# Performance work log

Hardware: AMD Instinct MI355X
Metric: run time of the kernel (lower is better)

## Reference

```python
import jax, jax.numpy as jnp
import numpy as np

D_MODEL, D_K, D_V, H = 1024, 64, 64, 16


def setup_inputs() -> dict:
    key = jax.random.key(0)
    ks = jax.random.split(key, 11)
    b, nq, nk = 2, 2048, 2048
    queries = jax.random.normal(ks[0], (b, nq, D_MODEL), dtype=jnp.float32)
    keys = jax.random.normal(ks[1], (b, nk, D_MODEL), dtype=jnp.float32)
    values = jax.random.normal(ks[2], (b, nk, D_MODEL), dtype=jnp.float32)
    def xavier(k, shape):
        fan_in, fan_out = shape[1], shape[0]
        lim = np.sqrt(6.0 / (fan_in + fan_out)).astype(np.float32)
        return jax.random.uniform(k, shape, jnp.float32, -lim, lim)
    # torch Linear weight shape: (out_features, in_features)
    Wq = xavier(ks[3], (H * D_K, D_MODEL)); bq = jnp.zeros((H * D_K,), jnp.float32)
    Wk = xavier(ks[4], (H * D_K, D_MODEL)); bk = jnp.zeros((H * D_K,), jnp.float32)
    Wv = xavier(ks[5], (H * D_V, D_MODEL)); bv = jnp.zeros((H * D_V,), jnp.float32)
    Wo = xavier(ks[6], (D_MODEL, H * D_V)); bo = jnp.zeros((D_MODEL,), jnp.float32)
    return {"queries": queries, "keys": keys, "values": values,
            "Wq": Wq, "bq": bq, "Wk": Wk, "bk": bk,
            "Wv": Wv, "bv": bv, "Wo": Wo, "bo": bo}


def reference(queries, keys, values, Wq, bq, Wk, bk, Wv, bv, Wo, bo):
    b, nq, _ = queries.shape
    nk = keys.shape[1]
    scale = 1.0 / np.sqrt(D_K).astype(np.float32)
    # projections -> (b, h, n, d)
    q = (queries @ Wq.T + bq).reshape(b, nq, H, D_K).transpose(0, 2, 1, 3)
    k = (keys @ Wk.T + bk).reshape(b, nk, H, D_K).transpose(0, 2, 1, 3)
    v = (values @ Wv.T + bv).reshape(b, nk, H, D_V).transpose(0, 2, 1, 3)
    att = jnp.einsum('bhqd,bhkd->bhqk', q, k) * scale  # (b,h,nq,nk)
    att = jax.nn.softmax(att, axis=-1)
    out = jnp.einsum('bhqk,bhkd->bhqd', att, v)        # (b,h,nq,dv)
    out = out.transpose(0, 2, 1, 3).reshape(b, nq, H * D_V)
    return out @ Wo.T + bo
```

## Files before the change

kernel.cpp:

```cpp
#include <hip/hip_runtime.h>
#include <stdint.h>

typedef __bf16 v8bf __attribute__((ext_vector_type(8)));
typedef float  v4f  __attribute__((ext_vector_type(4)));

#define QSCALE 0.18033688011112042f

typedef __attribute__((address_space(3))) void lds_vp;
typedef const __attribute__((address_space(1))) void gbl_vp;
__device__ __forceinline__ void gl_lds16(const __bf16* g, __bf16* l) {
    __builtin_amdgcn_global_load_lds((gbl_vp*)g, (lds_vp*)l, 16, 0, 0);
}

__device__ __forceinline__ v8bf cvt8(const float* __restrict__ p) {
    float4 x = *reinterpret_cast<const float4*>(p);
    float4 y = *reinterpret_cast<const float4*>(p + 4);
    v8bf r;
    r[0] = (__bf16)x.x; r[1] = (__bf16)x.y; r[2] = (__bf16)x.z; r[3] = (__bf16)x.w;
    r[4] = (__bf16)y.x; r[5] = (__bf16)y.y; r[6] = (__bf16)y.z; r[7] = (__bf16)y.w;
    return r;
}

__global__ __launch_bounds__(256) void cvt_w(
    const float* __restrict__ w0, const float* __restrict__ w1,
    const float* __restrict__ w2, const float* __restrict__ w3,
    __bf16* __restrict__ o0, __bf16* __restrict__ o1,
    __bf16* __restrict__ o2, __bf16* __restrict__ o3)
{
    const float* src; __bf16* dst;
    switch (blockIdx.y) {
        case 0: src = w0; dst = o0; break;
        case 1: src = w1; dst = o1; break;
        case 2: src = w2; dst = o2; break;
        default: src = w3; dst = o3; break;
    }
    size_t i = ((size_t)blockIdx.x * 256 + threadIdx.x) * 8;
    *reinterpret_cast<v8bf*>(dst + i) = cvt8(src + i);
}

__global__ __launch_bounds__(256) void cvt_in(
    const float* __restrict__ i0, const float* __restrict__ i1,
    const float* __restrict__ i2,
    __bf16* __restrict__ o0, __bf16* __restrict__ o1, __bf16* __restrict__ o2)
{
    const float* src; __bf16* dst;
    switch (blockIdx.y) {
        case 0: src = i0; dst = o0; break;
        case 1: src = i1; dst = o1; break;
        default: src = i2; dst = o2; break;
    }
    size_t i = ((size_t)blockIdx.x * 256 + threadIdx.x) * 8;
    *reinterpret_cast<v8bf*>(dst + i) = cvt8(src + i);
}

__device__ __forceinline__ void gemm_body(
    const __bf16* __restrict__ A, const __bf16* __restrict__ W,
    const float* __restrict__ bias, void* __restrict__ outp,
    int mode, float oscale, int bx, int by)
{
    constexpr int K = 1024, N = 1024;
    __shared__ __align__(16) __bf16 As[2][128 * 64];
    __shared__ __align__(16) __bf16 Bs[2][64 * 64];

    const int lane = threadIdx.x & 63;
    const int wave = threadIdx.x >> 6;
    const int quad = lane >> 4;
    const int l15  = lane & 15;
    const int m_base = bx * 128;
    const int n_base = by * 64;
    const int wm = (wave & 1) * 64;
    const int wn = (wave >> 1) * 32;

    int arow[4], acol[4], brow[2], bcol[2];
    #pragma unroll
    for (int i = 0; i < 4; ++i) {
        int L = (i * 4 + wave) * 64 + lane;
        int r = L >> 3, s = L & 7;
        arow[i] = r; acol[i] = (s ^ (r & 7)) * 8;
    }
    #pragma unroll
    for (int i = 0; i < 2; ++i) {
        int L = (i * 4 + wave) * 64 + lane;
        int r = L >> 3, s = L & 7;
        brow[i] = r; bcol[i] = (s ^ (r & 7)) * 8;
    }

    v4f acc[4][2];
    #pragma unroll
    for (int f = 0; f < 4; ++f)
        #pragma unroll
        for (int g = 0; g < 2; ++g) { v4f z = {0.f,0.f,0.f,0.f}; acc[f][g] = z; }

    #pragma unroll
    for (int i = 0; i < 4; ++i)
        gl_lds16(A + (size_t)(m_base + arow[i]) * K + acol[i],
                 &As[0][(i * 4 + wave) * 512]);
    #pragma unroll
    for (int i = 0; i < 2; ++i)
        gl_lds16(W + (size_t)(n_base + brow[i]) * K + bcol[i],
                 &Bs[0][(i * 4 + wave) * 512]);
    __syncthreads();

    for (int it = 0; it < 16; ++it) {
        const int cur = it & 1, nxt = cur ^ 1;
        const int kn = ((it + 1) & 15) * 64;
        #pragma unroll
        for (int i = 0; i < 4; ++i)
            gl_lds16(A + (size_t)(m_base + arow[i]) * K + kn + acol[i],
                     &As[nxt][(i * 4 + wave) * 512]);
        #pragma unroll
        for (int i = 0; i < 2; ++i)
            gl_lds16(W + (size_t)(n_base + brow[i]) * K + kn + bcol[i],
                     &Bs[nxt][(i * 4 + wave) * 512]);

        #pragma unroll
        for (int ks = 0; ks < 2; ++ks) {
            v8bf af[4], bf[2];
            #pragma unroll
            for (int f = 0; f < 4; ++f) {
                const int R = wm + f * 16 + l15;
                const int slot = (ks * 4 + quad) ^ (R & 7);
                af[f] = *reinterpret_cast<const v8bf*>(&As[cur][R * 64 + slot * 8]);
            }
            #pragma unroll
            for (int g = 0; g < 2; ++g) {
                const int R = wn + g * 16 + l15;
                const int slot = (ks * 4 + quad) ^ (R & 7);
                bf[g] = *reinterpret_cast<const v8bf*>(&Bs[cur][R * 64 + slot * 8]);
            }
            __builtin_amdgcn_s_setprio(1);
            #pragma unroll
            for (int f = 0; f < 4; ++f)
                #pragma unroll
                for (int g = 0; g < 2; ++g)
                    acc[f][g] = __builtin_amdgcn_mfma_f32_16x16x32_bf16(
                        af[f], bf[g], acc[f][g], 0, 0, 0);
            __builtin_amdgcn_s_setprio(0);
        }
        __syncthreads();
    }

    #pragma unroll
    for (int f = 0; f < 4; ++f)
        #pragma unroll
        for (int g = 0; g < 2; ++g) {
            const int nc = n_base + wn + g * 16 + l15;
            const float bval = bias[nc];
            #pragma unroll
            for (int r = 0; r < 4; ++r) {
                const int m = m_base + wm + f * 16 + quad * 4 + r;
                const float v = (acc[f][g][r] + bval) * oscale;
                if (mode == 2) {
                    ((float*)outp)[(size_t)m * N + nc] = v;
                } else {
                    int b = m >> 11, n = m & 2047, h = nc >> 6, d = nc & 63;
                    size_t off = (mode == 0)
                        ? ((size_t)(b * 16 + h) * 2048 + n) * 64 + d
                        : ((size_t)(b * 16 + h) * 64 + d) * 2048 + n;
                    ((__bf16*)outp)[off] = (__bf16)v;
                }
            }
        }
}

__global__ __launch_bounds__(256) void qkv_gemm(
    const __bf16* __restrict__ Aq, const __bf16* __restrict__ Ak,
    const __bf16* __restrict__ Av,
    const __bf16* __restrict__ Wq, const __bf16* __restrict__ Wk,
    const __bf16* __restrict__ Wv,
    const float* __restrict__ bq, const float* __restrict__ bk,
    const float* __restrict__ bv,
    __bf16* __restrict__ Qo, __bf16* __restrict__ Ko, __bf16* __restrict__ Vo)
{
    const int id = blockIdx.x;
    const int by = id & 15;
    const int bx = (id >> 4) & 31;
    const int z  = id >> 9;

    const __bf16 *A, *W; const float* bias; __bf16* outp; float oscale; int mode;
    switch (z) {
        case 0:  A = Aq; W = Wq; bias = bq; outp = Qo; oscale = QSCALE; mode = 0; break;
        case 1:  A = Ak; W = Wk; bias = bk; outp = Ko; oscale = 1.0f;   mode = 0; break;
        default: A = Av; W = Wv; bias = bv; outp = Vo; oscale = 1.0f;   mode = 1; break;
    }
    gemm_body(A, W, bias, outp, mode, oscale, bx, by);
}

__global__ __launch_bounds__(256) void out_gemm(
    const __bf16* __restrict__ A, const __bf16* __restrict__ W,
    const float* __restrict__ bias, float* __restrict__ outp)
{
    const int by = blockIdx.x & 15;
    const int bx = blockIdx.x >> 4;
    gemm_body(A, W, bias, outp, 2, 1.0f, bx, by);
}

__global__ __launch_bounds__(512, 4) void attn_kernel(
    const __bf16* __restrict__ Q, const __bf16* __restrict__ Kb_,
    const __bf16* __restrict__ Vt, __bf16* __restrict__ O)
{
    __shared__ __align__(16) __bf16 Ks[3][64 * 64];
    __shared__ __align__(16) __bf16 Vs[3][64 * 64];
    __shared__ __align__(16) __bf16 p_lds[8][16][72];

    const int lane = threadIdx.x & 63;
    const int wave = threadIdx.x >> 6;
    const int quad = lane >> 4;
    const int l15  = lane & 15;
    const int bh = blockIdx.x & 31;
    const int qt = blockIdx.x >> 5;
    const int b  = bh >> 4, h = bh & 15;

    const __bf16* Qh = Q   + (size_t)bh * 2048 * 64;
    const __bf16* Kh = Kb_ + (size_t)bh * 2048 * 64;
    const __bf16* Vh = Vt  + (size_t)bh * 64 * 2048;

    const int L    = wave * 64 + lane;
    const int srow = L >> 3;
    const int scol = ((L & 7) ^ (srow & 7)) * 8;

    v8bf qf[2];
    #pragma unroll
    for (int ks = 0; ks < 2; ++ks)
        qf[ks] = *reinterpret_cast<const v8bf*>(
            Qh + (size_t)(qt * 128 + wave * 16 + l15) * 64 + ks * 32 + quad * 8);

    v4f o_acc[4];
    #pragma unroll
    for (int c = 0; c < 4; ++c) { v4f z = {0.f,0.f,0.f,0.f}; o_acc[c] = z; }
    float l_r[4] = {0.f, 0.f, 0.f, 0.f};

    gl_lds16(Kh + (size_t)srow * 64 + scol, &Ks[0][L * 8]);
    gl_lds16(Vh + (size_t)srow * 2048 + scol, &Vs[0][L * 8]);
    gl_lds16(Kh + (size_t)(64 + srow) * 64 + scol, &Ks[1][L * 8]);
    gl_lds16(Vh + (size_t)srow * 2048 + 64 + scol, &Vs[1][L * 8]);
    asm volatile("s_waitcnt vmcnt(2)" ::: "memory");
    __builtin_amdgcn_s_barrier();

    int cur = 0;
    for (int kt = 0; kt < 32; ++kt) {
        int pre = cur + 2; if (pre >= 3) pre -= 3;
        int ktn = kt + 2; if (ktn >= 32) ktn -= 32;
        gl_lds16(Kh + (size_t)(ktn * 64 + srow) * 64 + scol, &Ks[pre][L * 8]);
        gl_lds16(Vh + (size_t)srow * 2048 + ktn * 64 + scol, &Vs[pre][L * 8]);

        v4f s_t[4];
        #pragma unroll
        for (int c = 0; c < 4; ++c) { v4f z = {0.f,0.f,0.f,0.f}; s_t[c] = z; }
        #pragma unroll
        for (int ks = 0; ks < 2; ++ks) {
            v8bf kf[4];
            #pragma unroll
            for (int c = 0; c < 4; ++c) {
                const int R = c * 16 + l15;
                const int slot = (ks * 4 + quad) ^ (R & 7);
                kf[c] = *reinterpret_cast<const v8bf*>(&Ks[cur][R * 64 + slot * 8]);
            }
            __builtin_amdgcn_s_setprio(1);
            #pragma unroll
            for (int c = 0; c < 4; ++c)
                s_t[c] = __builtin_amdgcn_mfma_f32_16x16x32_bf16(qf[ks], kf[c], s_t[c], 0, 0, 0);
            __builtin_amdgcn_s_setprio(0);
        }

        #pragma unroll
        for (int r = 0; r < 4; ++r) {
            const float p0 = __builtin_exp2f(s_t[0][r]);
            const float p1 = __builtin_exp2f(s_t[1][r]);
            const float p2 = __builtin_exp2f(s_t[2][r]);
            const float p3 = __builtin_exp2f(s_t[3][r]);
            l_r[r] += (p0 + p1) + (p2 + p3);
            p_lds[wave][quad * 4 + r][0 * 16 + l15] = (__bf16)p0;
            p_lds[wave][quad * 4 + r][1 * 16 + l15] = (__bf16)p1;
            p_lds[wave][quad * 4 + r][2 * 16 + l15] = (__bf16)p2;
            p_lds[wave][quad * 4 + r][3 * 16 + l15] = (__bf16)p3;
        }

        #pragma unroll
        for (int ks = 0; ks < 2; ++ks) {
            v8bf vf[4];
            #pragma unroll
            for (int c = 0; c < 4; ++c) {
                const int R = c * 16 + l15;
                const int slot = (ks * 4 + quad) ^ (R & 7);
                vf[c] = *reinterpret_cast<const v8bf*>(&Vs[cur][R * 64 + slot * 8]);
            }
            const v8bf pf = *reinterpret_cast<const v8bf*>(
                &p_lds[wave][l15][ks * 32 + quad * 8]);
            __builtin_amdgcn_s_setprio(1);
            #pragma unroll
            for (int c = 0; c < 4; ++c)
                o_acc[c] = __builtin_amdgcn_mfma_f32_16x16x32_bf16(pf, vf[c], o_acc[c], 0, 0, 0);
            __builtin_amdgcn_s_setprio(0);
        }

        asm volatile("s_waitcnt vmcnt(2)" ::: "memory");
        __builtin_amdgcn_s_barrier();
        cur = (cur == 2) ? 0 : cur + 1;
    }

    #pragma unroll
    for (int r = 0; r < 4; ++r) {
        float l = l_r[r];
        #pragma unroll
        for (int off = 1; off < 16; off <<= 1)
            l += __shfl_xor(l, off, 16);
        const float inv_l = 1.0f / l;
        const int qr = qt * 128 + wave * 16 + quad * 4 + r;
        #pragma unroll
        for (int c = 0; c < 4; ++c) {
            const int col = h * 64 + c * 16 + l15;
            O[(size_t)(b * 2048 + qr) * 1024 + col] = (__bf16)(o_acc[c][r] * inv_l);
        }
    }
}

extern "C" void kernel_launch(void* const* d_in, const int* in_sizes, int n_in,
                              void* d_out, int out_size, void* d_ws, size_t ws_size,
                              hipStream_t stream) {
    const float* q_in = (const float*)d_in[0];
    const float* k_in = (const float*)d_in[1];
    const float* v_in = (const float*)d_in[2];
    const float* Wq = (const float*)d_in[3];
    const float* bq = (const float*)d_in[4];
    const float* Wk = (const float*)d_in[5];
    const float* bk = (const float*)d_in[6];
    const float* Wv = (const float*)d_in[7];
    const float* bv = (const float*)d_in[8];
    const float* Wo = (const float*)d_in[9];
    const float* bo = (const float*)d_in[10];
    float* out = (float*)d_out;

    __bf16* ws  = (__bf16*)d_ws;
    __bf16* Abq = ws;
    __bf16* Abk = Abq + 4194304;
    __bf16* Abv = Abk + 4194304;
    __bf16* Qb  = Abv + 4194304;
    __bf16* Kb  = Qb  + 4194304;
    __bf16* Vb  = Kb  + 4194304;
    __bf16* Wqb = Vb  + 4194304;
    __bf16* Wkb = Wqb + 1048576;
    __bf16* Wvb = Wkb + 1048576;
    __bf16* Wob = Wvb + 1048576;
    __bf16* Ob  = Abq;

    cvt_w<<<dim3(512, 4), 256, 0, stream>>>(Wq, Wk, Wv, Wo, Wqb, Wkb, Wvb, Wob);
    cvt_in<<<dim3(2048, 3), 256, 0, stream>>>(q_in, k_in, v_in, Abq, Abk, Abv);

    qkv_gemm<<<1536, 256, 0, stream>>>(
        Abq, Abk, Abv, Wqb, Wkb, Wvb, bq, bk, bv, Qb, Kb, Vb);

    attn_kernel<<<512, 512, 0, stream>>>(Qb, Kb, Vb, Ob);

    out_gemm<<<512, 256, 0, stream>>>(Ob, Wob, bo, out);
}
```

Measured before the change: 246.0 us.

## Triple-buffer GEMM LDS pipeline and merge conversion kernels into one launch

The GEMM main loop moves from double to triple buffering in LDS. Tiles are prefetched two iterations ahead, and the full __syncthreads is replaced by a partial s_waitcnt vmcnt(6) plus a barrier, so the next tile's loads can stay in flight across iterations. Separately, the weight and input fp32-to-bf16 conversion kernels are merged into a single launch to remove one kernel launch. The triple buffer raises LDS usage from 48KB to 72KB per block, which may lower occupancy. The hand-written waitcnt relies on correct accounting of outstanding loads.

```diff
diff --git a/kernel.cpp b/kernel.cpp
--- a/kernel.cpp
+++ b/kernel.cpp
@@ -21,35 +21,36 @@
     return r;
 }
 
-__global__ __launch_bounds__(256) void cvt_w(
+__global__ __launch_bounds__(256) void cvt_all(
     const float* __restrict__ w0, const float* __restrict__ w1,
     const float* __restrict__ w2, const float* __restrict__ w3,
-    __bf16* __restrict__ o0, __bf16* __restrict__ o1,
-    __bf16* __restrict__ o2, __bf16* __restrict__ o3)
-{
-    const float* src; __bf16* dst;
-    switch (blockIdx.y) {
-        case 0: src = w0; dst = o0; break;
-        case 1: src = w1; dst = o1; break;
-        case 2: src = w2; dst = o2; break;
-        default: src = w3; dst = o3; break;
-    }
-    size_t i = ((size_t)blockIdx.x * 256 + threadIdx.x) * 8;
-    *reinterpret_cast<v8bf*>(dst + i) = cvt8(src + i);
-}
-
-__global__ __launch_bounds__(256) void cvt_in(
     const float* __restrict__ i0, const float* __restrict__ i1,
     const float* __restrict__ i2,
-    __bf16* __restrict__ o0, __bf16* __restrict__ o1, __bf16* __restrict__ o2)
-{
-    const float* src; __bf16* dst;
-    switch (blockIdx.y) {
-        case 0: src = i0; dst = o0; break;
-        case 1: src = i1; dst = o1; break;
-        default: src = i2; dst = o2; break;
-    }
-    size_t i = ((size_t)blockIdx.x * 256 + threadIdx.x) * 8;
+    __bf16* __restrict__ ow0, __bf16* __restrict__ ow1,
+    __bf16* __restrict__ ow2, __bf16* __restrict__ ow3,
+    __bf16* __restrict__ oi0, __bf16* __restrict__ oi1,
+    __bf16* __restrict__ oi2)
+{
+    const int id = blockIdx.x;
+    const float* src; __bf16* dst; int blk;
+    if (id < 2048) {
+        switch (id >> 9) {
+            case 0: src = w0; dst = ow0; break;
+            case 1: src = w1; dst = ow1; break;
+            case 2: src = w2; dst = ow2; break;
+            default: src = w3; dst = ow3; break;
+        }
+        blk = id & 511;
+    } else {
+        const int j = id - 2048;
+        switch (j >> 11) {
+            case 0: src = i0; dst = oi0; break;
+            case 1: src = i1; dst = oi1; break;
+            default: src = i2; dst = oi2; break;
+        }
+        blk = j & 2047;
+    }
+    size_t i = ((size_t)blk * 256 + threadIdx.x) * 8;
     *reinterpret_cast<v8bf*>(dst + i) = cvt8(src + i);
 }
 
@@ -59,8 +60,8 @@
     int mode, float oscale, int bx, int by)
 {
     constexpr int K = 1024, N = 1024;
-    __shared__ __align__(16) __bf16 As[2][128 * 64];
-    __shared__ __align__(16) __bf16 Bs[2][64 * 64];
+    __shared__ __align__(16) __bf16 As[3][128 * 64];
+    __shared__ __align__(16) __bf16 Bs[3][64 * 64];
 
     const int lane = threadIdx.x & 63;
     const int wave = threadIdx.x >> 6;
@@ -99,19 +100,29 @@
     for (int i = 0; i < 2; ++i)
         gl_lds16(W + (size_t)(n_base + brow[i]) * K + bcol[i],
                  &Bs[0][(i * 4 + wave) * 512]);
-    __syncthreads();
-
+    #pragma unroll
+    for (int i = 0; i < 4; ++i)
+        gl_lds16(A + (size_t)(m_base + arow[i]) * K + 64 + acol[i],
+                 &As[1][(i * 4 + wave) * 512]);
+    #pragma unroll
+    for (int i = 0; i < 2; ++i)
+        gl_lds16(W + (size_t)(n_base + brow[i]) * K + 64 + bcol[i],
+                 &Bs[1][(i * 4 + wave) * 512]);
+    asm volatile("s_waitcnt vmcnt(6)" ::: "memory");
+    __builtin_amdgcn_s_barrier();
+
+    int cur = 0;
     for (int it = 0; it < 16; ++it) {
-        const int cur = it & 1, nxt = cur ^ 1;
-        const int kn = ((it + 1) & 15) * 64;
+        int pre = cur + 2; if (pre >= 3) pre -= 3;
+        const int kn = ((it + 2) & 15) * 64;
         #pragma unroll
         for (int i = 0; i < 4; ++i)
             gl_lds16(A + (size_t)(m_base + arow[i]) * K + kn + acol[i],
-                     &As[nxt][(i * 4 + wave) * 512]);
+                     &As[pre][(i * 4 + wave) * 512]);
         #pragma unroll
         for (int i = 0; i < 2; ++i)
             gl_lds16(W + (size_t)(n_base + brow[i]) * K + kn + bcol[i],
-                     &Bs[nxt][(i * 4 + wave) * 512]);
+                     &Bs[pre][(i * 4 + wave) * 512]);
 
         #pragma unroll
         for (int ks = 0; ks < 2; ++ks) {
@@ -137,7 +148,10 @@
                         af[f], bf[g], acc[f][g], 0, 0, 0);
             __builtin_amdgcn_s_setprio(0);
         }
-        __syncthreads();
+
+        asm volatile("s_waitcnt vmcnt(6)" ::: "memory");
+        __builtin_amdgcn_s_barrier();
+        cur = (cur == 2) ? 0 : cur + 1;
     }
 
     #pragma unroll
@@ -344,8 +358,8 @@
     __bf16* Wob = Wvb + 1048576;
     __bf16* Ob  = Abq;
 
-    cvt_w<<<dim3(512, 4), 256, 0, stream>>>(Wq, Wk, Wv, Wo, Wqb, Wkb, Wvb, Wob);
-    cvt_in<<<dim3(2048, 3), 256, 0, stream>>>(q_in, k_in, v_in, Abq, Abk, Abv);
+    cvt_all<<<8192, 256, 0, stream>>>(Wq, Wk, Wv, Wo, q_in, k_in, v_in,
+                                      Wqb, Wkb, Wvb, Wob, Abq, Abk, Abv);
 
     qkv_gemm<<<1536, 256, 0, stream>>>(
         Abq, Abk, Abv, Wqb, Wkb, Wvb, bq, bk, bv, Qb, Kb, Vb);
```

Measured after the change: 254.0 us. 1.03x slower.
